# Kernel tuning notes

Hardware: AMD Instinct MI355X
Metric: run time of the kernel (lower is better)

Reference implementation:

```python
import jax, jax.numpy as jnp
import numpy as np

V_ORIG = 32000   # original embedding vocab
V_NEW = 8000     # reparameterized vocab (size of down/up stacks and index_mapping)
D = 1024         # embedding dim
R = 16           # low-rank dim
N = 16384        # number of indices looked up


def setup_inputs() -> dict:
    key = jax.random.key(0)
    k1, k2, k3, k4, k5 = jax.random.split(key, 5)
    indices = jax.random.randint(k1, (N,), 0, V_NEW, dtype=jnp.int64)
    # index_mapping: dict new_index -> original_index, materialized as a lookup array
    index_map = jax.random.randint(k2, (V_NEW,), 0, V_ORIG, dtype=jnp.int64)
    emb_weight = jax.random.normal(k3, (V_ORIG, D), dtype=jnp.float32) * 0.02
    down = jax.random.normal(k4, (V_NEW, D, R), dtype=jnp.float32) * (1.0 / np.sqrt(D))
    up = jax.random.normal(k5, (V_NEW, R, D), dtype=jnp.float32) * (1.0 / np.sqrt(R))
    return {"indices": indices, "index_map": index_map,
            "emb_weight": emb_weight, "down": down, "up": up}


def reference(indices, index_map, emb_weight, down, up):
    # Gather original embeddings via the index mapping: [N, D]
    e = emb_weight[index_map[indices]]
    # Per-index low-rank projection: ([1,D] @ [D,R]) @ [R,D], batched over N
    h = jnp.einsum('nd,ndr->nr', e, down[indices])        # [N, R]
    out = jnp.einsum('nr,nrd->nd', h, up[indices])        # [N, D]
    # Original stacks per-index [1, D] results -> [N, 1, D]
    return out[:, None, :]
```

## Files before the change

kernel.cpp:

```cpp
#include <hip/hip_runtime.h>
#include <hip/hip_bf16.h>


#define DDIM 1024
#define RDIM 16

typedef float v4f __attribute__((ext_vector_type(4)));

static __device__ __forceinline__ v4f ldnt(const float* p) {
    return __builtin_nontemporal_load((const v4f*)p);
}
static __device__ __forceinline__ void stnt(float* p, v4f v) {
    __builtin_nontemporal_store(v, (v4f*)p);
}
static __device__ __forceinline__ v4f sel4(bool c, v4f a, v4f b) {
    v4f r;
    r[0] = c ? a[0] : b[0];
    r[1] = c ? a[1] : b[1];
    r[2] = c ? a[2] : b[2];
    r[3] = c ? a[3] : b[3];
    return r;
}

__global__ __launch_bounds__(256) void link_kernel(const int* __restrict__ idx,
                                                   int* __restrict__ head,
                                                   int* __restrict__ next,
                                                   int* __restrict__ work,
                                                   int* __restrict__ nwork, int n) {
    int i = blockIdx.x * 256 + threadIdx.x;
    if (i < n) {
        int v = idx[i];
        int old = atomicExch(&head[v], i);
        next[i] = old;
        if (old < 0) work[atomicAdd(nwork, 1)] = v;
    }
}

static __device__ __forceinline__ void compute_row(
    const float* __restrict__ e_lds,
    const float* __restrict__ dn,
    const float* __restrict__ u,
    int lane, v4f& a0, v4f& a1, v4f& a2, v4f& a3)
{
    const int c0   = lane & 3;
    const int dgrp = lane >> 2;

    v4f hp = {0.f, 0.f, 0.f, 0.f};
    const float* dnb = dn + (dgrp << 4) + (c0 << 2);
    #pragma unroll 8
    for (int k = 0; k < 64; ++k) {
        const float ed = e_lds[(k << 4) + dgrp];
        const v4f dq = ldnt(dnb + (k << 8));
        hp += ed * dq;
    }

    #pragma unroll
    for (int m = 4; m < 64; m <<= 1) {
        v4f t;
        t[0] = __shfl_xor(hp[0], m, 64);
        t[1] = __shfl_xor(hp[1], m, 64);
        t[2] = __shfl_xor(hp[2], m, 64);
        t[3] = __shfl_xor(hp[3], m, 64);
        hp += t;
    }

    v4f t1;
    t1[0] = __shfl_xor(hp[0], 1, 64);
    t1[1] = __shfl_xor(hp[1], 1, 64);
    t1[2] = __shfl_xor(hp[2], 1, 64);
    t1[3] = __shfl_xor(hp[3], 1, 64);
    const bool odd = (c0 & 1) != 0;
    v4f pe = sel4(odd, t1, hp);
    v4f po = sel4(odd, hp, t1);
    v4f pe2, po2;
    pe2[0] = __shfl_xor(pe[0], 2, 64);
    pe2[1] = __shfl_xor(pe[1], 2, 64);
    pe2[2] = __shfl_xor(pe[2], 2, 64);
    pe2[3] = __shfl_xor(pe[3], 2, 64);
    po2[0] = __shfl_xor(po[0], 2, 64);
    po2[1] = __shfl_xor(po[1], 2, 64);
    po2[2] = __shfl_xor(po[2], 2, 64);
    po2[3] = __shfl_xor(po[3], 2, 64);
    const bool hi = (c0 & 2) != 0;
    const v4f q0 = sel4(hi, pe2, pe);
    const v4f q2 = sel4(hi, pe, pe2);
    const v4f q1 = sel4(hi, po2, po);
    const v4f q3 = sel4(hi, po, po2);

    float hh[16];
    #pragma unroll
    for (int i = 0; i < 4; ++i) {
        hh[i]      = q0[i];
        hh[4 + i]  = q1[i];
        hh[8 + i]  = q2[i];
        hh[12 + i] = q3[i];
    }

    a0 = (v4f){0.f, 0.f, 0.f, 0.f};
    a1 = a0; a2 = a0; a3 = a0;
    const float* ub = u + (lane << 2);
    #pragma unroll 4
    for (int r = 0; r < RDIM; ++r) {
        const float* ur = ub + (r << 10);
        const v4f u0 = ldnt(ur + 0);
        const v4f u1 = ldnt(ur + 256);
        const v4f u2 = ldnt(ur + 512);
        const v4f u3 = ldnt(ur + 768);
        const float hf = hh[r];
        a0 += hf * u0;
        a1 += hf * u1;
        a2 += hf * u2;
        a3 += hf * u3;
    }
}

__global__ __launch_bounds__(256) void fused_wave_kernel(
    const int* __restrict__ index_map,
    const float* __restrict__ emb,
    const float* __restrict__ down,
    const float* __restrict__ up,
    const int* __restrict__ head,
    const int* __restrict__ next,
    const int* __restrict__ work,
    const int* __restrict__ nwork,
    float* __restrict__ out)
{
    __shared__ v4f els4[4][DDIM / 4];
    const int lane = threadIdx.x & 63;
    const int wib  = threadIdx.x >> 6;
    const int wi   = (blockIdx.x << 2) | wib;
    if (wi >= *nwork) return;
    const int v = work[wi];

    const v4f* e4 = (const v4f*)(emb + (size_t)index_map[v] * DDIM);
    els4[wib][lane]       = e4[lane];
    els4[wib][lane + 64]  = e4[lane + 64];
    els4[wib][lane + 128] = e4[lane + 128];
    els4[wib][lane + 192] = e4[lane + 192];
    const float* e_lds = (const float*)&els4[wib][0];

    v4f a0, a1, a2, a3;
    compute_row(e_lds,
                down + (size_t)v * (DDIM * RDIM),
                up   + (size_t)v * (RDIM * DDIM),
                lane, a0, a1, a2, a3);

    int n = head[v];
    while (n >= 0) {
        float* o = out + (size_t)n * DDIM + (lane << 2);
        stnt(o + 0,   a0);
        stnt(o + 256, a1);
        stnt(o + 512, a2);
        stnt(o + 768, a3);
        n = next[n];
    }
}

__global__ __launch_bounds__(256) void rows_direct_kernel(
    const int* __restrict__ indices,
    const int* __restrict__ index_map,
    const float* __restrict__ emb,
    const float* __restrict__ down,
    const float* __restrict__ up,
    float* __restrict__ out, int N)
{
    __shared__ v4f els4[4][DDIM / 4];
    const int lane = threadIdx.x & 63;
    const int wib  = threadIdx.x >> 6;
    const int nn   = (blockIdx.x << 2) | wib;
    if (nn >= N) return;
    const int v = indices[nn];

    const v4f* e4 = (const v4f*)(emb + (size_t)index_map[v] * DDIM);
    els4[wib][lane]       = e4[lane];
    els4[wib][lane + 64]  = e4[lane + 64];
    els4[wib][lane + 128] = e4[lane + 128];
    els4[wib][lane + 192] = e4[lane + 192];
    const float* e_lds = (const float*)&els4[wib][0];

    v4f a0, a1, a2, a3;
    compute_row(e_lds,
                down + (size_t)v * (DDIM * RDIM),
                up   + (size_t)v * (RDIM * DDIM),
                lane, a0, a1, a2, a3);

    float* o = out + (size_t)nn * DDIM + (lane << 2);
    stnt(o + 0,   a0);
    stnt(o + 256, a1);
    stnt(o + 512, a2);
    stnt(o + 768, a3);
}

extern "C" void kernel_launch(void* const* d_in, const int* in_sizes, int n_in,
                              void* d_out, int out_size, void* d_ws, size_t ws_size,
                              hipStream_t stream)
{
    const int*   indices   = (const int*)d_in[0];
    const int*   index_map = (const int*)d_in[1];
    const float* emb       = (const float*)d_in[2];
    const float* down      = (const float*)d_in[3];
    const float* up        = (const float*)d_in[4];
    float*       out       = (float*)d_out;

    const int N = in_sizes[0];
    const int V = in_sizes[1];

    const size_t ws_need = (size_t)(2 * V + N + 1) * sizeof(int);

    if (ws_size >= ws_need) {
        int* head  = (int*)d_ws;
        int* next  = head + V;
        int* work  = next + N;
        int* nwork = work + V;
        hipMemsetAsync(head, 0xFF, (size_t)V * sizeof(int), stream);
        hipMemsetAsync(nwork, 0x00, sizeof(int), stream);
        link_kernel<<<(N + 255) / 256, 256, 0, stream>>>(indices, head, next, work, nwork, N);
        fused_wave_kernel<<<(V + 3) / 4, 256, 0, stream>>>(index_map, emb, down, up,
                                                           head, next, work, nwork, out);
    } else {
        rows_direct_kernel<<<(N + 3) / 4, 256, 0, stream>>>(indices, index_map, emb,
                                                            down, up, out, N);
    }
}
```

Before: 194.8 us.

## Split fused row kernel into separate down-projection and up-projection kernels

Replaces the single fused per-unique-index kernel with two grid-stride kernels. The first computes the rank-16 h vector for each unique index into workspace, and the second reads h, applies the up projection and scatters the result to every duplicate output row. The intent is to separate the two memory-bound phases so each kernel has a simpler access pattern and fewer registers, and to use a fixed grid of 1024 blocks. This costs an extra launch, a small h round-trip through global memory, and a larger workspace requirement.

```diff
diff --git a/kernel.cpp b/kernel.cpp
--- a/kernel.cpp
+++ b/kernel.cpp
@@ -12,14 +12,6 @@
 }
 static __device__ __forceinline__ void stnt(float* p, v4f v) {
     __builtin_nontemporal_store(v, (v4f*)p);
-}
-static __device__ __forceinline__ v4f sel4(bool c, v4f a, v4f b) {
-    v4f r;
-    r[0] = c ? a[0] : b[0];
-    r[1] = c ? a[1] : b[1];
-    r[2] = c ? a[2] : b[2];
-    r[3] = c ? a[3] : b[3];
-    return r;
 }
 
 __global__ __launch_bounds__(256) void link_kernel(const int* __restrict__ idx,
@@ -36,24 +28,155 @@
     }
 }
 
-static __device__ __forceinline__ void compute_row(
-    const float* __restrict__ e_lds,
-    const float* __restrict__ dn,
-    const float* __restrict__ u,
-    int lane, v4f& a0, v4f& a1, v4f& a2, v4f& a3)
-{
+__global__ __launch_bounds__(256) void h_kernel(
+    const int* __restrict__ index_map,
+    const float* __restrict__ emb,
+    const float* __restrict__ down,
+    const int* __restrict__ work,
+    const int* __restrict__ nwork,
+    float* __restrict__ h)
+{
+    __shared__ v4f els4[4][DDIM / 4];
+    const int lane = threadIdx.x & 63;
+    const int wib  = threadIdx.x >> 6;
+    const int nw   = *nwork;
+    const int stride = gridDim.x << 2;
+
+    for (int wi = (blockIdx.x << 2) + wib; wi < nw; wi += stride) {
+        const int v = work[wi];
+
+        const v4f* e4 = (const v4f*)(emb + (size_t)index_map[v] * DDIM);
+        els4[wib][lane]       = e4[lane];
+        els4[wib][lane + 64]  = e4[lane + 64];
+        els4[wib][lane + 128] = e4[lane + 128];
+        els4[wib][lane + 192] = e4[lane + 192];
+        const float* e_lds = (const float*)&els4[wib][0];
+
+        const int c0   = lane & 3;
+        const int dgrp = lane >> 2;
+        const float* dnb = down + (size_t)v * (DDIM * RDIM) + (dgrp << 4) + (c0 << 2);
+
+        v4f hp = {0.f, 0.f, 0.f, 0.f};
+        #pragma unroll 8
+        for (int k = 0; k < 64; ++k) {
+            const float ed = e_lds[(k << 4) + dgrp];
+            const v4f dq = ldnt(dnb + (k << 8));
+            hp += ed * dq;
+        }
+
+        #pragma unroll
+        for (int m = 4; m < 64; m <<= 1) {
+            v4f t;
+            t[0] = __shfl_xor(hp[0], m, 64);
+            t[1] = __shfl_xor(hp[1], m, 64);
+            t[2] = __shfl_xor(hp[2], m, 64);
+            t[3] = __shfl_xor(hp[3], m, 64);
+            hp += t;
+        }
+
+        if (lane < 4)
+            *(v4f*)(h + (size_t)wi * RDIM + (lane << 2)) = hp;
+    }
+}
+
+__global__ __launch_bounds__(256) void out_kernel(
+    const float* __restrict__ up,
+    const int* __restrict__ head,
+    const int* __restrict__ next,
+    const int* __restrict__ work,
+    const int* __restrict__ nwork,
+    const float* __restrict__ h,
+    float* __restrict__ out)
+{
+    const int lane = threadIdx.x & 63;
+    const int wib  = threadIdx.x >> 6;
+    const int nw   = *nwork;
+    const int stride = gridDim.x << 2;
+
+    for (int wi = (blockIdx.x << 2) + wib; wi < nw; wi += stride) {
+        const int v = work[wi];
+
+        const v4f* hv = (const v4f*)(h + (size_t)wi * RDIM);
+        const v4f h0 = hv[0], h1 = hv[1], h2 = hv[2], h3 = hv[3];
+        float hh[16];
+        #pragma unroll
+        for (int i = 0; i < 4; ++i) {
+            hh[i]      = h0[i];
+            hh[4 + i]  = h1[i];
+            hh[8 + i]  = h2[i];
+            hh[12 + i] = h3[i];
+        }
+
+        v4f a0 = {0.f, 0.f, 0.f, 0.f}, a1 = a0, a2 = a0, a3 = a0;
+        const float* ub = up + (size_t)v * (RDIM * DDIM) + (lane << 2);
+        #pragma unroll 4
+        for (int r = 0; r < RDIM; ++r) {
+            const float* ur = ub + (r << 10);
+            const v4f u0 = ldnt(ur + 0);
+            const v4f u1 = ldnt(ur + 256);
+            const v4f u2 = ldnt(ur + 512);
+            const v4f u3 = ldnt(ur + 768);
+            const float hf = hh[r];
+            a0 += hf * u0;
+            a1 += hf * u1;
+            a2 += hf * u2;
+            a3 += hf * u3;
+        }
+
+        int n = head[v];
+        while (n >= 0) {
+            float* o = out + (size_t)n * DDIM + (lane << 2);
+            stnt(o + 0,   a0);
+            stnt(o + 256, a1);
+            stnt(o + 512, a2);
+            stnt(o + 768, a3);
+            n = next[n];
+        }
+    }
+}
+
+static __device__ __forceinline__ v4f sel4(bool c, v4f a, v4f b) {
+    v4f r;
+    r[0] = c ? a[0] : b[0];
+    r[1] = c ? a[1] : b[1];
+    r[2] = c ? a[2] : b[2];
+    r[3] = c ? a[3] : b[3];
+    return r;
+}
+
+__global__ __launch_bounds__(256) void rows_direct_kernel(
+    const int* __restrict__ indices,
+    const int* __restrict__ index_map,
+    const float* __restrict__ emb,
+    const float* __restrict__ down,
+    const float* __restrict__ up,
+    float* __restrict__ out, int N)
+{
+    __shared__ v4f els4[4][DDIM / 4];
+    const int lane = threadIdx.x & 63;
+    const int wib  = threadIdx.x >> 6;
+    const int nn   = (blockIdx.x << 2) | wib;
+    if (nn >= N) return;
+    const int v = indices[nn];
+
+    const v4f* e4 = (const v4f*)(emb + (size_t)index_map[v] * DDIM);
+    els4[wib][lane]       = e4[lane];
+    els4[wib][lane + 64]  = e4[lane + 64];
+    els4[wib][lane + 128] = e4[lane + 128];
+    els4[wib][lane + 192] = e4[lane + 192];
+    const float* e_lds = (const float*)&els4[wib][0];
+
     const int c0   = lane & 3;
     const int dgrp = lane >> 2;
+    const float* dnb = down + (size_t)v * (DDIM * RDIM) + (dgrp << 4) + (c0 << 2);
 
     v4f hp = {0.f, 0.f, 0.f, 0.f};
-    const float* dnb = dn + (dgrp << 4) + (c0 << 2);
     #pragma unroll 8
     for (int k = 0; k < 64; ++k) {
         const float ed = e_lds[(k << 4) + dgrp];
         const v4f dq = ldnt(dnb + (k << 8));
         hp += ed * dq;
     }
-
     #pragma unroll
     for (int m = 4; m < 64; m <<= 1) {
         v4f t;
@@ -63,7 +186,6 @@
         t[3] = __shfl_xor(hp[3], m, 64);
         hp += t;
     }
-
     v4f t1;
     t1[0] = __shfl_xor(hp[0], 1, 64);
     t1[1] = __shfl_xor(hp[1], 1, 64);
@@ -96,9 +218,8 @@
         hh[12 + i] = q3[i];
     }
 
-    a0 = (v4f){0.f, 0.f, 0.f, 0.f};
-    a1 = a0; a2 = a0; a3 = a0;
-    const float* ub = u + (lane << 2);
+    v4f a0 = {0.f, 0.f, 0.f, 0.f}, a1 = a0, a2 = a0, a3 = a0;
+    const float* ub = up + (size_t)v * (RDIM * DDIM) + (lane << 2);
     #pragma unroll 4
     for (int r = 0; r < RDIM; ++r) {
         const float* ur = ub + (r << 10);
@@ -112,78 +233,6 @@
         a2 += hf * u2;
         a3 += hf * u3;
     }
-}
-
-__global__ __launch_bounds__(256) void fused_wave_kernel(
-    const int* __restrict__ index_map,
-    const float* __restrict__ emb,
-    const float* __restrict__ down,
-    const float* __restrict__ up,
-    const int* __restrict__ head,
-    const int* __restrict__ next,
-    const int* __restrict__ work,
-    const int* __restrict__ nwork,
-    float* __restrict__ out)
-{
-    __shared__ v4f els4[4][DDIM / 4];
-    const int lane = threadIdx.x & 63;
-    const int wib  = threadIdx.x >> 6;
-    const int wi   = (blockIdx.x << 2) | wib;
-    if (wi >= *nwork) return;
-    const int v = work[wi];
-
-    const v4f* e4 = (const v4f*)(emb + (size_t)index_map[v] * DDIM);
-    els4[wib][lane]       = e4[lane];
-    els4[wib][lane + 64]  = e4[lane + 64];
-    els4[wib][lane + 128] = e4[lane + 128];
-    els4[wib][lane + 192] = e4[lane + 192];
-    const float* e_lds = (const float*)&els4[wib][0];
-
-    v4f a0, a1, a2, a3;
-    compute_row(e_lds,
-                down + (size_t)v * (DDIM * RDIM),
-                up   + (size_t)v * (RDIM * DDIM),
-                lane, a0, a1, a2, a3);
-
-    int n = head[v];
-    while (n >= 0) {
-        float* o = out + (size_t)n * DDIM + (lane << 2);
-        stnt(o + 0,   a0);
-        stnt(o + 256, a1);
-        stnt(o + 512, a2);
-        stnt(o + 768, a3);
-        n = next[n];
-    }
-}
-
-__global__ __launch_bounds__(256) void rows_direct_kernel(
-    const int* __restrict__ indices,
-    const int* __restrict__ index_map,
-    const float* __restrict__ emb,
-    const float* __restrict__ down,
-    const float* __restrict__ up,
-    float* __restrict__ out, int N)
-{
-    __shared__ v4f els4[4][DDIM / 4];
-    const int lane = threadIdx.x & 63;
-    const int wib  = threadIdx.x >> 6;
-    const int nn   = (blockIdx.x << 2) | wib;
-    if (nn >= N) return;
-    const int v = indices[nn];
-
-    const v4f* e4 = (const v4f*)(emb + (size_t)index_map[v] * DDIM);
-    els4[wib][lane]       = e4[lane];
-    els4[wib][lane + 64]  = e4[lane + 64];
-    els4[wib][lane + 128] = e4[lane + 128];
-    els4[wib][lane + 192] = e4[lane + 192];
-    const float* e_lds = (const float*)&els4[wib][0];
-
-    v4f a0, a1, a2, a3;
-    compute_row(e_lds,
-                down + (size_t)v * (DDIM * RDIM),
-                up   + (size_t)v * (RDIM * DDIM),
-                lane, a0, a1, a2, a3);
-
     float* o = out + (size_t)nn * DDIM + (lane << 2);
     stnt(o + 0,   a0);
     stnt(o + 256, a1);
@@ -205,18 +254,20 @@
     const int N = in_sizes[0];
     const int V = in_sizes[1];
 
-    const size_t ws_need = (size_t)(2 * V + N + 1) * sizeof(int);
+    const size_t ws_need = (size_t)V * RDIM * sizeof(float)
+                         + (size_t)(2 * V + N + 1) * sizeof(int);
 
     if (ws_size >= ws_need) {
-        int* head  = (int*)d_ws;
-        int* next  = head + V;
-        int* work  = next + N;
-        int* nwork = work + V;
+        float* h     = (float*)d_ws;
+        int*   head  = (int*)(h + (size_t)V * RDIM);
+        int*   next  = head + V;
+        int*   work  = next + N;
+        int*   nwork = work + V;
         hipMemsetAsync(head, 0xFF, (size_t)V * sizeof(int), stream);
         hipMemsetAsync(nwork, 0x00, sizeof(int), stream);
         link_kernel<<<(N + 255) / 256, 256, 0, stream>>>(indices, head, next, work, nwork, N);
-        fused_wave_kernel<<<(V + 3) / 4, 256, 0, stream>>>(index_map, emb, down, up,
-                                                           head, next, work, nwork, out);
+        h_kernel<<<1024, 256, 0, stream>>>(index_map, emb, down, work, nwork, h);
+        out_kernel<<<1024, 256, 0, stream>>>(up, head, next, work, nwork, h, out);
     } else {
         rows_direct_kernel<<<(N + 3) / 4, 256, 0, stream>>>(indices, index_map, emb,
                                                             down, up, out, N);
```

Result: faster. 185.6 us, median of 2 (-4.7%).
